# Performance work log

Measured on AMD Instinct MI355X. Metric: run time of the kernel, lower is better.

Reference implementation:

```python
import jax, jax.numpy as jnp
import numpy as np

H, DH = 8, 64  # num_heads, head_dim


def setup_inputs() -> dict:
    key = jax.random.key(0)
    ks = jax.random.split(key, 7)
    m, nq, nkv, d = 4, 2048, 2048, 512
    return {
        "xq": jax.random.normal(ks[0], (m, nq, d), jnp.float32),
        "xk": jax.random.normal(ks[1], (m, nkv, d), jnp.float32),
        "xv": jax.random.normal(ks[2], (m, nkv, d), jnp.float32),
        "Wq": jax.random.normal(ks[3], (d, H * DH), jnp.float32) * 0.02,
        "Wk": jax.random.normal(ks[4], (d, H * DH), jnp.float32) * 0.02,
        "Wv": jax.random.normal(ks[5], (d, H * DH), jnp.float32) * 0.02,
        "Wo": jax.random.normal(ks[6], (H * DH, d), jnp.float32) * 0.02,
        "bo": jnp.zeros((d,), jnp.float32),
    }


def _split_heads(t):
    # [b, n, h*d] -> [b, h, n, d]
    b, n, _ = t.shape
    return t.reshape(b, n, H, DH).transpose(0, 2, 1, 3)


def reference(xq, xk, xv, Wq, Wk, Wv, Wo, bo):
    scale = DH ** -0.5
    q = _split_heads(xq @ Wq)   # [b,h,nq,dh]
    k = _split_heads(xk @ Wk)   # [b,h,nkv,dh]
    v = _split_heads(xv @ Wv)   # [b,h,nkv,dh]
    dots = jnp.einsum("bhqd,bhkd->bhqk", q, k) * scale  # [b,h,nq,nkv]
    # diagonal attention term: query attends to its own (k,v) projection
    xq_k = _split_heads(xq @ Wk)
    xq_v = _split_heads(xq @ Wv)
    diag = jnp.sum(q * xq_k, axis=-1, keepdims=True) * scale  # [b,h,nq,1]
    dots = jnp.concatenate([dots, diag], axis=-1)  # [b,h,nq,nkv+1]
    attn = jax.nn.softmax(dots, axis=-1)
    out = jnp.einsum("bhqk,bhkd->bhqd", attn[..., :-1], v) + attn[..., -1:] * xq_v
    b, _, nq, _ = out.shape
    out = out.transpose(0, 2, 1, 3).reshape(b, nq, H * DH)  # merge heads
    return out @ Wo + bo
```

## Files before the change

### kernel.cpp

```cpp
#include <hip/hip_runtime.h>

#define LOG2E 1.44269504088896f
#define CS (0.125f * LOG2E)

typedef __bf16 bf16x8 __attribute__((ext_vector_type(8)));
typedef float f32x4 __attribute__((ext_vector_type(4)));
typedef unsigned short u16x8 __attribute__((ext_vector_type(8)));

#if __has_builtin(__builtin_amdgcn_exp2f)
#define fexp2(x) __builtin_amdgcn_exp2f(x)
#else
extern "C" __device__ float __ocml_native_exp2_f32(float);
#define fexp2(x) __ocml_native_exp2_f32(x)
#endif

__device__ __forceinline__ unsigned short f2bf(float f) {
  union { float f; unsigned int u; } v{f};
  unsigned int r = v.u + 0x7fffu + ((v.u >> 16) & 1u);
  return (unsigned short)(r >> 16);
}
__device__ __forceinline__ float bf2f(unsigned short u) {
  union { unsigned int u; float f; } v; v.u = ((unsigned int)u) << 16; return v.f;
}
__device__ __forceinline__ unsigned int pkr(float a, float b) {
  unsigned int ua = __builtin_bit_cast(unsigned int, a) + 0x8000u;
  unsigned int ub = __builtin_bit_cast(unsigned int, b) + 0x8000u;
  return __builtin_amdgcn_perm(ub, ua, 0x07060302);
}

typedef __attribute__((address_space(3))) unsigned int lds32_t;
typedef const __attribute__((address_space(1))) unsigned int glb32_t;
__device__ __forceinline__ void gld16(const unsigned short* g, unsigned short* l) {
  __builtin_amdgcn_global_load_lds((glb32_t*)(unsigned long long)g,
                                   (lds32_t*)(unsigned int)(unsigned long long)l,
                                   16, 0, 0);
}

__global__ __launch_bounds__(256) void conv_all(
    const float* __restrict__ xq, const float* __restrict__ xk, const float* __restrict__ xv,
    const float* __restrict__ Wq, const float* __restrict__ Wk,
    const float* __restrict__ Wv, const float* __restrict__ Wo,
    unsigned short* __restrict__ oxq, unsigned short* __restrict__ oxk, unsigned short* __restrict__ oxv,
    unsigned short* __restrict__ oWq, unsigned short* __restrict__ oWk,
    unsigned short* __restrict__ oWv, unsigned short* __restrict__ oWo) {
  __shared__ unsigned short T[64 * 65];
  const int blk = blockIdx.x;
  if (blk < 12288) {
    const int N4 = (8192 * 512) / 4;
    int idx = blk * 256 + threadIdx.x;
    const float* src; unsigned short* dst; int i;
    if (idx < N4)          { src = xq; dst = oxq; i = idx; }
    else if (idx < 2 * N4) { src = xk; dst = oxk; i = idx - N4; }
    else                   { src = xv; dst = oxv; i = idx - 2 * N4; }
    float4 v = ((const float4*)src)[i];
    ushort4 o; o.x = f2bf(v.x); o.y = f2bf(v.y); o.z = f2bf(v.z); o.w = f2bf(v.w);
    ((ushort4*)dst)[i] = o;
  } else {
    const int wblk = blk - 12288;
    const int wsel = wblk >> 6;
    const int tile = wblk & 63;
    const int tk = (tile >> 3) * 64, tn = (tile & 7) * 64;
    const float* src = (wsel == 0) ? Wq : (wsel == 1) ? Wk : (wsel == 2) ? Wv : Wo;
    unsigned short* dst = (wsel == 0) ? oWq : (wsel == 1) ? oWk : (wsel == 2) ? oWv : oWo;
    const float scale = (wsel == 0) ? CS : 1.0f;
    const int rr = threadIdx.x >> 4;
    const int cc = (threadIdx.x & 15) * 4;
#pragma unroll
    for (int i = 0; i < 4; i++) {
      int row = rr + i * 16;
      float4 v = *(const float4*)&src[(size_t)(tk + row) * 512 + tn + cc];
      T[(cc + 0) * 65 + row] = f2bf(v.x * scale);
      T[(cc + 1) * 65 + row] = f2bf(v.y * scale);
      T[(cc + 2) * 65 + row] = f2bf(v.z * scale);
      T[(cc + 3) * 65 + row] = f2bf(v.w * scale);
    }
    __syncthreads();
#pragma unroll
    for (int i = 0; i < 4; i++) {
      int n = rr + i * 16;
      ushort4 o;
      o.x = T[n * 65 + cc + 0]; o.y = T[n * 65 + cc + 1];
      o.z = T[n * 65 + cc + 2]; o.w = T[n * 65 + cc + 3];
      *(ushort4*)&dst[(size_t)(tn + n) * 512 + tk + cc] = o;
    }
  }
}

__device__ __forceinline__ void gemm_tile(
    const unsigned short* __restrict__ A, const unsigned short* __restrict__ Bt,
    int rowBlk, int colBlk, unsigned short* As, unsigned short* Bs, f32x4 (&acc)[4][4]) {
  const int t = threadIdx.x;
  const int lane = t & 63, c = lane & 15, g = lane >> 4;
  const int w = t >> 6;
  const int wm = w & 1, wn = w >> 1;
#pragma unroll
  for (int i = 0; i < 4; i++)
#pragma unroll
    for (int j = 0; j < 4; j++)
#pragma unroll
      for (int r = 0; r < 4; r++) acc[i][j][r] = 0.f;

  const int sr = t >> 2, sch = t & 3;
#define STAGE_PROJ(kkk, buf)                                                     \
  do {                                                                           \
    unsigned short* Ad = As + (buf) * (128 * 32);                                \
    unsigned short* Bd = Bs + (buf) * (128 * 32);                                \
    gld16(&A[(size_t)(rowBlk + sr) * 512 + (kkk) + sch * 8], &Ad[t * 8]);        \
    gld16(&Bt[(size_t)(colBlk + sr) * 512 + (kkk) + sch * 8], &Bd[t * 8]);       \
    gld16(&A[(size_t)(rowBlk + sr + 64) * 512 + (kkk) + sch * 8],                \
          &Ad[(t + 256) * 8]);                                                   \
    gld16(&Bt[(size_t)(colBlk + sr + 64) * 512 + (kkk) + sch * 8],               \
          &Bd[(t + 256) * 8]);                                                   \
  } while (0)

  STAGE_PROJ(0, 0);
  __syncthreads();

  for (int kt = 0; kt < 16; kt++) {
    if (kt < 15) STAGE_PROJ((kt + 1) * 32, (kt + 1) & 1);
    const unsigned short* Ac = As + (kt & 1) * (128 * 32);
    const unsigned short* Bc = Bs + (kt & 1) * (128 * 32);
    bf16x8 af[4], bfr[4];
#pragma unroll
    for (int i = 0; i < 4; i++)
      af[i] = __builtin_bit_cast(bf16x8, *(const u16x8*)&Ac[(wm * 64 + i * 16 + c) * 32 + g * 8]);
#pragma unroll
    for (int j = 0; j < 4; j++)
      bfr[j] = __builtin_bit_cast(bf16x8, *(const u16x8*)&Bc[(wn * 64 + j * 16 + c) * 32 + g * 8]);
#pragma unroll
    for (int i = 0; i < 4; i++)
#pragma unroll
      for (int j = 0; j < 4; j++)
        acc[i][j] = __builtin_amdgcn_mfma_f32_16x16x32_bf16(af[i], bfr[j], acc[i][j], 0, 0, 0);
    if (kt < 15) __syncthreads();
  }
#undef STAGE_PROJ
}

__global__ __launch_bounds__(256) void proj_all(
    const unsigned short* __restrict__ xq, const unsigned short* __restrict__ xk,
    const unsigned short* __restrict__ xv,
    const unsigned short* __restrict__ Wq, const unsigned short* __restrict__ Wk,
    const unsigned short* __restrict__ Wv,
    unsigned short* __restrict__ Qo, unsigned short* __restrict__ XKo,
    unsigned short* __restrict__ XVo, unsigned short* __restrict__ Ko,
    unsigned short* __restrict__ Vto) {
  __shared__ unsigned short As[2 * 128 * 32];
  __shared__ unsigned short Bs[2 * 128 * 32];
  const int rowBlk = blockIdx.x * 128;
  const int y = blockIdx.y;
  const unsigned short* A; const unsigned short* Bt; int colBlk; int mode;
  unsigned short* out;
  if (y < 12) {
    int wsel = y >> 2;
    A = xq; colBlk = (y & 3) * 128; mode = 0;
    Bt = (wsel == 0) ? Wq : (wsel == 1) ? Wk : Wv;
    out = (wsel == 0) ? Qo : (wsel == 1) ? XKo : XVo;
  } else if (y < 16) {
    A = xk; Bt = Wk; out = Ko; colBlk = (y - 12) * 128; mode = 0;
  } else {
    A = xv; Bt = Wv; out = Vto; colBlk = (y - 16) * 128; mode = 1;
  }
  f32x4 acc[4][4];
  gemm_tile(A, Bt, rowBlk, colBlk, As, Bs, acc);
  const int t = threadIdx.x;
  const int w = t >> 6, lane = t & 63, c = lane & 15, g = lane >> 4;
  const int wm = w & 1, wn = w >> 1;
  if (mode == 0) {
#pragma unroll
    for (int i = 0; i < 4; i++)
#pragma unroll
      for (int j = 0; j < 4; j++)
#pragma unroll
        for (int r = 0; r < 4; r++) {
          int row = rowBlk + wm * 64 + i * 16 + g * 4 + r;
          int col = colBlk + wn * 64 + j * 16 + c;
          out[(size_t)row * 512 + col] = f2bf(acc[i][j][r]);
        }
  } else {
#pragma unroll
    for (int i = 0; i < 4; i++) {
      int tok0 = rowBlk + wm * 64 + i * 16 + g * 4;
      int bb = tok0 >> 11, n0 = tok0 & 2047;
#pragma unroll
      for (int j = 0; j < 4; j++) {
        int col = colBlk + wn * 64 + j * 16 + c;
        int hh = col >> 6, dh = col & 63;
        ushort4 o;
        o.x = f2bf(acc[i][j][0]); o.y = f2bf(acc[i][j][1]);
        o.z = f2bf(acc[i][j][2]); o.w = f2bf(acc[i][j][3]);
        *(ushort4*)&out[((size_t)(bb * 8 + hh) * 64 + dh) * 2048 + n0] = o;
      }
    }
  }
}

__global__ __launch_bounds__(256) void gemm_out(
    const unsigned short* __restrict__ A, const unsigned short* __restrict__ Bt,
    float* __restrict__ out, const float* __restrict__ bias) {
  __shared__ unsigned short As[2 * 128 * 32];
  __shared__ unsigned short Bs[2 * 64 * 32];
  const int rowBlk = blockIdx.x * 128;
  const int colBlk = blockIdx.y * 64;
  const int t = threadIdx.x;
  const int lane = t & 63, c = lane & 15, g = lane >> 4;
  const int w = t >> 6;
  const int wm = w & 1, wn = w >> 1;
  f32x4 acc[4][2];
#pragma unroll
  for (int i = 0; i < 4; i++)
#pragma unroll
    for (int j = 0; j < 2; j++)
#pragma unroll
      for (int r = 0; r < 4; r++) acc[i][j][r] = 0.f;

  const int sr = t >> 2, sch = t & 3;
#define STAGE_OUT(kkk, buf)                                                      \
  do {                                                                           \
    unsigned short* Ad = As + (buf) * (128 * 32);                                \
    unsigned short* Bd = Bs + (buf) * (64 * 32);                                 \
    gld16(&A[(size_t)(rowBlk + sr) * 512 + (kkk) + sch * 8], &Ad[t * 8]);        \
    gld16(&A[(size_t)(rowBlk + sr + 64) * 512 + (kkk) + sch * 8],                \
          &Ad[(t + 256) * 8]);                                                   \
    gld16(&Bt[(size_t)(colBlk + sr) * 512 + (kkk) + sch * 8], &Bd[t * 8]);       \
  } while (0)

  STAGE_OUT(0, 0);
  __syncthreads();

  for (int kt = 0; kt < 16; kt++) {
    if (kt < 15) STAGE_OUT((kt + 1) * 32, (kt + 1) & 1);
    const unsigned short* Ac = As + (kt & 1) * (128 * 32);
    const unsigned short* Bc = Bs + (kt & 1) * (64 * 32);
    bf16x8 af[4], bfr[2];
#pragma unroll
    for (int i = 0; i < 4; i++)
      af[i] = __builtin_bit_cast(bf16x8, *(const u16x8*)&Ac[(wm * 64 + i * 16 + c) * 32 + g * 8]);
#pragma unroll
    for (int j = 0; j < 2; j++)
      bfr[j] = __builtin_bit_cast(bf16x8, *(const u16x8*)&Bc[(wn * 32 + j * 16 + c) * 32 + g * 8]);
#pragma unroll
    for (int i = 0; i < 4; i++)
#pragma unroll
      for (int j = 0; j < 2; j++)
        acc[i][j] = __builtin_amdgcn_mfma_f32_16x16x32_bf16(af[i], bfr[j], acc[i][j], 0, 0, 0);
    if (kt < 15) __syncthreads();
  }
#undef STAGE_OUT
#pragma unroll
  for (int i = 0; i < 4; i++)
#pragma unroll
    for (int j = 0; j < 2; j++)
#pragma unroll
      for (int r = 0; r < 4; r++) {
        int row = rowBlk + wm * 64 + i * 16 + g * 4 + r;
        int col = colBlk + wn * 32 + j * 16 + c;
        out[(size_t)row * 512 + col] = acc[i][j][r] + bias[col];
      }
}

__global__ __launch_bounds__(512, 4) void attn_kernel(
    const unsigned short* __restrict__ Q, const unsigned short* __restrict__ K,
    const unsigned short* __restrict__ Vt, const unsigned short* __restrict__ XK,
    const unsigned short* __restrict__ XV, unsigned short* __restrict__ O) {
  __shared__ unsigned short Ks[2][64 * 64];
  __shared__ unsigned short Vs[3][64 * 64];
  __shared__ unsigned short Ps[2][8][16 * 72];
  __shared__ float Scr[8][32];
  const int t = threadIdx.x;
  const int w = t >> 6, lane = t & 63, c = lane & 15, g = lane >> 4;
  const int id = blockIdx.x + 16 * (blockIdx.y + 8 * blockIdx.z);
  const int h = id & 7;
  const int jj = id >> 3;
  const int qt = jj & 15;
  const int b = jj >> 4;
  const size_t hb = (size_t)b * (2048 * 512) + h * 64;
  const size_t vhb = (size_t)(b * 8 + h) * 64 * 2048;
  const int qbase = qt * 128 + w * 16;

  const int sr = t >> 3, sch = t & 7;
  const int ssl = (sch ^ (sr & 7)) * 8;
  const size_t kgoff = hb + (size_t)sr * 512 + ssl;
  const size_t vgoff = vhb + (size_t)sr * 2048 + ssl;

  const int sw0 = ((g ^ (c & 7)) << 3);
  const int sw1 = (((g | 4) ^ (c & 7)) << 3);

  bf16x8 qf[2];
#pragma unroll
  for (int hf = 0; hf < 2; hf++)
    qf[hf] = __builtin_bit_cast(bf16x8,
        *(const u16x8*)&Q[hb + (size_t)(qbase + c) * 512 + hf * 32 + g * 8]);

  f32x4 accO[4];
  float lq = 0.f;
#pragma unroll
  for (int jd = 0; jd < 4; jd++)
#pragma unroll
    for (int r = 0; r < 4; r++) accO[jd][r] = 0.f;

  gld16(&K[kgoff], &Ks[0][t * 8]);
  gld16(&Vt[vgoff], &Vs[0][t * 8]);
  __syncthreads();

  gld16(&K[kgoff + (size_t)(64 * 512)], &Ks[1][t * 8]);
  gld16(&Vt[vgoff + 64], &Vs[1][t * 8]);
  {
    unsigned short* Pw = &Ps[0][w][0];
    f32x4 s[4];
    __builtin_amdgcn_s_setprio(1);
#pragma unroll
    for (int j = 0; j < 4; j++) {
      bf16x8 kf0 = __builtin_bit_cast(bf16x8, *(const u16x8*)&Ks[0][(j * 16 + c) * 64 + sw0]);
      bf16x8 kf1 = __builtin_bit_cast(bf16x8, *(const u16x8*)&Ks[0][(j * 16 + c) * 64 + sw1]);
      f32x4 z; z[0] = z[1] = z[2] = z[3] = 0.f;
      z = __builtin_amdgcn_mfma_f32_16x16x32_bf16(kf0, qf[0], z, 0, 0, 0);
      z = __builtin_amdgcn_mfma_f32_16x16x32_bf16(kf1, qf[1], z, 0, 0, 0);
      s[j] = z;
    }
    __builtin_amdgcn_s_setprio(0);
    float sum = 0.f;
#pragma unroll
    for (int j = 0; j < 4; j++) {
      float p0 = fexp2(s[j][0]);
      float p1 = fexp2(s[j][1]);
      float p2 = fexp2(s[j][2]);
      float p3 = fexp2(s[j][3]);
      sum += (p0 + p1) + (p2 + p3);
      uint2 pw; pw.x = pkr(p0, p1); pw.y = pkr(p2, p3);
      *(uint2*)&Pw[c * 72 + j * 16 + g * 4] = pw;
    }
    lq += sum;
  }
  __syncthreads();

  int vprev = 0, vcur = 1, vnext = 2;
  for (int kt = 1; kt < 32; kt++) {
    if (kt < 31) {
      gld16(&K[kgoff + (size_t)(kt + 1) * (64 * 512)], &Ks[(kt + 1) & 1][t * 8]);
      gld16(&Vt[vgoff + (size_t)(kt + 1) * 64], &Vs[vnext][t * 8]);
    }
    const unsigned short* Pp = &Ps[(kt - 1) & 1][w][0];
    bf16x8 pf0 = __builtin_bit_cast(bf16x8, *(const u16x8*)&Pp[c * 72 + g * 8]);
    bf16x8 pf1 = __builtin_bit_cast(bf16x8, *(const u16x8*)&Pp[c * 72 + 32 + g * 8]);

    const unsigned short* Kc = &Ks[kt & 1][0];
    f32x4 s[4];
    __builtin_amdgcn_s_setprio(1);
#pragma unroll
    for (int j = 0; j < 4; j++) {
      bf16x8 kf0 = __builtin_bit_cast(bf16x8, *(const u16x8*)&Kc[(j * 16 + c) * 64 + sw0]);
      bf16x8 kf1 = __builtin_bit_cast(bf16x8, *(const u16x8*)&Kc[(j * 16 + c) * 64 + sw1]);
      f32x4 z; z[0] = z[1] = z[2] = z[3] = 0.f;
      z = __builtin_amdgcn_mfma_f32_16x16x32_bf16(kf0, qf[0], z, 0, 0, 0);
      z = __builtin_amdgcn_mfma_f32_16x16x32_bf16(kf1, qf[1], z, 0, 0, 0);
      s[j] = z;
    }
    const unsigned short* Vc = &Vs[vprev][0];
#pragma unroll
    for (int jd = 0; jd < 4; jd++) {
      bf16x8 v0 = __builtin_bit_cast(bf16x8, *(const u16x8*)&Vc[(jd * 16 + c) * 64 + sw0]);
      bf16x8 v1 = __builtin_bit_cast(bf16x8, *(const u16x8*)&Vc[(jd * 16 + c) * 64 + sw1]);
      accO[jd] = __builtin_amdgcn_mfma_f32_16x16x32_bf16(pf0, v0, accO[jd], 0, 0, 0);
      accO[jd] = __builtin_amdgcn_mfma_f32_16x16x32_bf16(pf1, v1, accO[jd], 0, 0, 0);
    }
    __builtin_amdgcn_s_setprio(0);

    {
      unsigned short* Pw = &Ps[kt & 1][w][0];
      float sum = 0.f;
#pragma unroll
      for (int j = 0; j < 4; j++) {
        float p0 = fexp2(s[j][0]);
        float p1 = fexp2(s[j][1]);
        float p2 = fexp2(s[j][2]);
        float p3 = fexp2(s[j][3]);
        sum += (p0 + p1) + (p2 + p3);
        uint2 pw; pw.x = pkr(p0, p1); pw.y = pkr(p2, p3);
        *(uint2*)&Pw[c * 72 + j * 16 + g * 4] = pw;
      }
      lq += sum;
    }

    if (kt < 31) __syncthreads();
    int tmp = vprev; vprev = vcur; vcur = vnext; vnext = tmp;
  }

  {
    const unsigned short* Pp = &Ps[1][w][0];
    bf16x8 pf0 = __builtin_bit_cast(bf16x8, *(const u16x8*)&Pp[c * 72 + g * 8]);
    bf16x8 pf1 = __builtin_bit_cast(bf16x8, *(const u16x8*)&Pp[c * 72 + 32 + g * 8]);
    const unsigned short* Vc = &Vs[vprev][0];
    __builtin_amdgcn_s_setprio(1);
#pragma unroll
    for (int jd = 0; jd < 4; jd++) {
      bf16x8 v0 = __builtin_bit_cast(bf16x8, *(const u16x8*)&Vc[(jd * 16 + c) * 64 + sw0]);
      bf16x8 v1 = __builtin_bit_cast(bf16x8, *(const u16x8*)&Vc[(jd * 16 + c) * 64 + sw1]);
      accO[jd] = __builtin_amdgcn_mfma_f32_16x16x32_bf16(pf0, v0, accO[jd], 0, 0, 0);
      accO[jd] = __builtin_amdgcn_mfma_f32_16x16x32_bf16(pf1, v1, accO[jd], 0, 0, 0);
    }
    __builtin_amdgcn_s_setprio(0);
  }

  lq += __shfl_xor(lq, 16);
  lq += __shfl_xor(lq, 32);

  {
    const int qc = qbase + c;
    float part = 0.f;
    {
      const unsigned short* qp = &Q[hb + (size_t)qc * 512 + g * 16];
      const unsigned short* xp = &XK[hb + (size_t)qc * 512 + g * 16];
      u16x8 q0 = *(const u16x8*)&qp[0], q1 = *(const u16x8*)&qp[8];
      u16x8 x0 = *(const u16x8*)&xp[0], x1 = *(const u16x8*)&xp[8];
#pragma unroll
      for (int ii = 0; ii < 8; ii++)
        part += bf2f(q0[ii]) * bf2f(x0[ii]) + bf2f(q1[ii]) * bf2f(x1[ii]);
    }
    part += __shfl_xor(part, 16);
    part += __shfl_xor(part, 32);
    float pd = fexp2(part);
    float inv = 1.f / (lq + pd);
    if (g == 0) {
      Scr[w][c] = inv;
      Scr[w][16 + c] = pd * inv;
    }
    __builtin_amdgcn_s_waitcnt(0);
    f32x4 a4 = *(const f32x4*)&Scr[w][g * 4];
    f32x4 p4 = *(const f32x4*)&Scr[w][16 + g * 4];
#pragma unroll
    for (int jd = 0; jd < 4; jd++)
#pragma unroll
      for (int r = 0; r < 4; r++) {
        int qr = qbase + g * 4 + r;
        float xv = bf2f(XV[hb + (size_t)qr * 512 + jd * 16 + c]);
        float val = accO[jd][r] * a4[r] + p4[r] * xv;
        O[((size_t)(b * 2048 + qr)) * 512 + h * 64 + jd * 16 + c] = f2bf(val);
      }
  }
}

extern "C" void kernel_launch(void* const* d_in, const int* in_sizes, int n_in,
                              void* d_out, int out_size, void* d_ws, size_t ws_size,
                              hipStream_t stream) {
  const float* xq = (const float*)d_in[0];
  const float* xk = (const float*)d_in[1];
  const float* xv = (const float*)d_in[2];
  const float* Wq = (const float*)d_in[3];
  const float* Wk = (const float*)d_in[4];
  const float* Wv = (const float*)d_in[5];
  const float* Wo = (const float*)d_in[6];
  const float* bo = (const float*)d_in[7];

  unsigned short* ws = (unsigned short*)d_ws;
  const size_t MD = 8192ull * 512;
  const size_t WD = 512ull * 512;
  unsigned short* xq_b = ws;
  unsigned short* xk_b = xq_b + MD;
  unsigned short* xv_b = xk_b + MD;
  unsigned short* Wq_t = xv_b + MD;
  unsigned short* Wk_t = Wq_t + WD;
  unsigned short* Wv_t = Wk_t + WD;
  unsigned short* Wo_t = Wv_t + WD;
  unsigned short* Qb  = Wo_t + WD;
  unsigned short* Kb  = Qb + MD;
  unsigned short* Vtb = Kb + MD;
  unsigned short* XKb = Vtb + MD;
  unsigned short* XVb = XKb + MD;
  unsigned short* Ob  = XVb + MD;

  conv_all<<<dim3(12544), 256, 0, stream>>>(xq, xk, xv, Wq, Wk, Wv, Wo,
                                            xq_b, xk_b, xv_b, Wq_t, Wk_t, Wv_t, Wo_t);
  proj_all<<<dim3(64, 20), 256, 0, stream>>>(xq_b, xk_b, xv_b, Wq_t, Wk_t, Wv_t,
                                             Qb, XKb, XVb, Kb, Vtb);
  attn_kernel<<<dim3(16, 8, 4), 512, 0, stream>>>(Qb, Kb, Vtb, XKb, XVb, Ob);
  gemm_out<<<dim3(64, 8), 256, 0, stream>>>(Ob, Wo_t, (float*)d_out, bo);
}
```

Before: 202.4 us.

## Switch attention to 32x32 MFMA with register-resident P via permlane32 swap

Rewrites the attention kernel to use 32x32x16 bf16 MFMA, with each wave handling 32 query rows. The kernel now covers 256 queries per block, giving 256 blocks instead of 512. The P matrix stays in registers and is reshuffled with v_permlane32_swap instead of passing through LDS. This drops the software-pipelined P buffer and the triple-buffered V, removing LDS round trips and raising work per wave. The cost is more registers (launch bounds lowered to 2), less overlap of QK and PV, and only 256 blocks, which may underfill the GPU.

```diff
diff --git a/kernel.cpp b/kernel.cpp
--- a/kernel.cpp
+++ b/kernel.cpp
@@ -5,6 +5,7 @@
 
 typedef __bf16 bf16x8 __attribute__((ext_vector_type(8)));
 typedef float f32x4 __attribute__((ext_vector_type(4)));
+typedef float f32x16 __attribute__((ext_vector_type(16)));
 typedef unsigned short u16x8 __attribute__((ext_vector_type(8)));
 
 #if __has_builtin(__builtin_amdgcn_exp2f)
@@ -27,6 +28,8 @@
   unsigned int ub = __builtin_bit_cast(unsigned int, b) + 0x8000u;
   return __builtin_amdgcn_perm(ub, ua, 0x07060302);
 }
+
+#define PLSWAP(x, y) asm("v_permlane32_swap_b32 %0, %1" : "+v"(x), "+v"(y))
 
 typedef __attribute__((address_space(3))) unsigned int lds32_t;
 typedef const __attribute__((address_space(1))) unsigned int glb32_t;
@@ -259,185 +262,147 @@
       }
 }
 
-__global__ __launch_bounds__(512, 4) void attn_kernel(
+__global__ __launch_bounds__(512, 2) void attn_kernel(
     const unsigned short* __restrict__ Q, const unsigned short* __restrict__ K,
     const unsigned short* __restrict__ Vt, const unsigned short* __restrict__ XK,
     const unsigned short* __restrict__ XV, unsigned short* __restrict__ O) {
   __shared__ unsigned short Ks[2][64 * 64];
-  __shared__ unsigned short Vs[3][64 * 64];
-  __shared__ unsigned short Ps[2][8][16 * 72];
-  __shared__ float Scr[8][32];
+  __shared__ unsigned short Vs[2][64 * 64];
+  __shared__ float Fin[8][2][32];
   const int t = threadIdx.x;
-  const int w = t >> 6, lane = t & 63, c = lane & 15, g = lane >> 4;
-  const int id = blockIdx.x + 16 * (blockIdx.y + 8 * blockIdx.z);
-  const int h = id & 7;
-  const int jj = id >> 3;
-  const int qt = jj & 15;
-  const int b = jj >> 4;
+  const int w = t >> 6, lane = t & 63;
+  const int rowA = lane & 31, hi = lane >> 5, l7 = lane & 7;
+  const int id = blockIdx.x;
+  const int h = id & 7, qt = (id >> 3) & 7, b = id >> 6;
   const size_t hb = (size_t)b * (2048 * 512) + h * 64;
   const size_t vhb = (size_t)(b * 8 + h) * 64 * 2048;
-  const int qbase = qt * 128 + w * 16;
+  const int qb0 = qt * 256 + w * 32;
 
   const int sr = t >> 3, sch = t & 7;
   const int ssl = (sch ^ (sr & 7)) * 8;
   const size_t kgoff = hb + (size_t)sr * 512 + ssl;
   const size_t vgoff = vhb + (size_t)sr * 2048 + ssl;
 
-  const int sw0 = ((g ^ (c & 7)) << 3);
-  const int sw1 = (((g | 4) ^ (c & 7)) << 3);
-
-  bf16x8 qf[2];
-#pragma unroll
-  for (int hf = 0; hf < 2; hf++)
-    qf[hf] = __builtin_bit_cast(bf16x8,
-        *(const u16x8*)&Q[hb + (size_t)(qbase + c) * 512 + hf * 32 + g * 8]);
-
-  f32x4 accO[4];
+  bf16x8 qf[4];
+#pragma unroll
+  for (int d = 0; d < 4; d++)
+    qf[d] = __builtin_bit_cast(bf16x8,
+        *(const u16x8*)&Q[hb + (size_t)(qb0 + rowA) * 512 + d * 16 + hi * 8]);
+
+  f32x16 accO[2];
+#pragma unroll
+  for (int n = 0; n < 2; n++)
+#pragma unroll
+    for (int r = 0; r < 16; r++) accO[n][r] = 0.f;
   float lq = 0.f;
-#pragma unroll
-  for (int jd = 0; jd < 4; jd++)
-#pragma unroll
-    for (int r = 0; r < 4; r++) accO[jd][r] = 0.f;
 
   gld16(&K[kgoff], &Ks[0][t * 8]);
   gld16(&Vt[vgoff], &Vs[0][t * 8]);
   __syncthreads();
 
-  gld16(&K[kgoff + (size_t)(64 * 512)], &Ks[1][t * 8]);
-  gld16(&Vt[vgoff + 64], &Vs[1][t * 8]);
+  for (int kt = 0; kt < 32; kt++) {
+    const int cb = kt & 1;
+    if (kt < 31) {
+      gld16(&K[kgoff + (size_t)(kt + 1) * (64 * 512)], &Ks[cb ^ 1][t * 8]);
+      gld16(&Vt[vgoff + (size_t)(kt + 1) * 64], &Vs[cb ^ 1][t * 8]);
+    }
+    const unsigned short* Kc = &Ks[cb][0];
+    const unsigned short* Vc = &Vs[cb][0];
+
+    f32x16 s0, s1;
+#pragma unroll
+    for (int r = 0; r < 16; r++) { s0[r] = 0.f; s1[r] = 0.f; }
+    __builtin_amdgcn_s_setprio(1);
+#pragma unroll
+    for (int d = 0; d < 4; d++) {
+      bf16x8 k0 = __builtin_bit_cast(bf16x8,
+          *(const u16x8*)&Kc[rowA * 64 + (((d * 2 + hi) ^ l7) * 8)]);
+      s0 = __builtin_amdgcn_mfma_f32_32x32x16_bf16(k0, qf[d], s0, 0, 0, 0);
+    }
+#pragma unroll
+    for (int d = 0; d < 4; d++) {
+      bf16x8 k1 = __builtin_bit_cast(bf16x8,
+          *(const u16x8*)&Kc[(32 + rowA) * 64 + (((d * 2 + hi) ^ l7) * 8)]);
+      s1 = __builtin_amdgcn_mfma_f32_32x32x16_bf16(k1, qf[d], s1, 0, 0, 0);
+    }
+    __builtin_amdgcn_s_setprio(0);
+
+    float sum = 0.f;
+#pragma unroll
+    for (int r = 0; r < 16; r++) { s0[r] = fexp2(s0[r]); sum += s0[r]; }
+#pragma unroll
+    for (int r = 0; r < 16; r++) { s1[r] = fexp2(s1[r]); sum += s1[r]; }
+    lq += sum;
+
+#define PVSUB(P, T2)                                                            \
+  {                                                                             \
+    unsigned int x0 = pkr(P[0], P[1]),   y0 = pkr(P[4], P[5]);                  \
+    unsigned int x1 = pkr(P[2], P[3]),   y1 = pkr(P[6], P[7]);                  \
+    unsigned int x2 = pkr(P[8], P[9]),   y2 = pkr(P[12], P[13]);                \
+    unsigned int x3 = pkr(P[10], P[11]), y3 = pkr(P[14], P[15]);                \
+    PLSWAP(x0, y0); PLSWAP(x1, y1); PLSWAP(x2, y2); PLSWAP(x3, y3);             \
+    uint4 w0 = {x0, x1, y0, y1};                                                \
+    uint4 w1 = {x2, x3, y2, y3};                                                \
+    bf16x8 pa0 = __builtin_bit_cast(bf16x8, w0);                                \
+    bf16x8 pa1 = __builtin_bit_cast(bf16x8, w1);                                \
+    _Pragma("unroll")                                                           \
+    for (int n = 0; n < 2; n++) {                                               \
+      bf16x8 v0 = __builtin_bit_cast(bf16x8,                                    \
+          *(const u16x8*)&Vc[(n * 32 + rowA) * 64 + ((((T2) * 4 + hi) ^ l7) * 8)]); \
+      bf16x8 v1 = __builtin_bit_cast(bf16x8,                                    \
+          *(const u16x8*)&Vc[(n * 32 + rowA) * 64 + ((((T2) * 4 + 2 + hi) ^ l7) * 8)]); \
+      accO[n] = __builtin_amdgcn_mfma_f32_32x32x16_bf16(pa0, v0, accO[n], 0, 0, 0); \
+      accO[n] = __builtin_amdgcn_mfma_f32_32x32x16_bf16(pa1, v1, accO[n], 0, 0, 0); \
+    }                                                                           \
+  }
+    __builtin_amdgcn_s_setprio(1);
+    PVSUB(s0, 0);
+    PVSUB(s1, 1);
+    __builtin_amdgcn_s_setprio(0);
+#undef PVSUB
+
+    if (kt < 31) __syncthreads();
+  }
+
+  lq += __shfl_xor(lq, 32);
+
+  float part = 0.f;
   {
-    unsigned short* Pw = &Ps[0][w][0];
-    f32x4 s[4];
-    __builtin_amdgcn_s_setprio(1);
-#pragma unroll
-    for (int j = 0; j < 4; j++) {
-      bf16x8 kf0 = __builtin_bit_cast(bf16x8, *(const u16x8*)&Ks[0][(j * 16 + c) * 64 + sw0]);
-      bf16x8 kf1 = __builtin_bit_cast(bf16x8, *(const u16x8*)&Ks[0][(j * 16 + c) * 64 + sw1]);
-      f32x4 z; z[0] = z[1] = z[2] = z[3] = 0.f;
-      z = __builtin_amdgcn_mfma_f32_16x16x32_bf16(kf0, qf[0], z, 0, 0, 0);
-      z = __builtin_amdgcn_mfma_f32_16x16x32_bf16(kf1, qf[1], z, 0, 0, 0);
-      s[j] = z;
-    }
-    __builtin_amdgcn_s_setprio(0);
-    float sum = 0.f;
-#pragma unroll
-    for (int j = 0; j < 4; j++) {
-      float p0 = fexp2(s[j][0]);
-      float p1 = fexp2(s[j][1]);
-      float p2 = fexp2(s[j][2]);
-      float p3 = fexp2(s[j][3]);
-      sum += (p0 + p1) + (p2 + p3);
-      uint2 pw; pw.x = pkr(p0, p1); pw.y = pkr(p2, p3);
-      *(uint2*)&Pw[c * 72 + j * 16 + g * 4] = pw;
-    }
-    lq += sum;
-  }
-  __syncthreads();
-
-  int vprev = 0, vcur = 1, vnext = 2;
-  for (int kt = 1; kt < 32; kt++) {
-    if (kt < 31) {
-      gld16(&K[kgoff + (size_t)(kt + 1) * (64 * 512)], &Ks[(kt + 1) & 1][t * 8]);
-      gld16(&Vt[vgoff + (size_t)(kt + 1) * 64], &Vs[vnext][t * 8]);
-    }
-    const unsigned short* Pp = &Ps[(kt - 1) & 1][w][0];
-    bf16x8 pf0 = __builtin_bit_cast(bf16x8, *(const u16x8*)&Pp[c * 72 + g * 8]);
-    bf16x8 pf1 = __builtin_bit_cast(bf16x8, *(const u16x8*)&Pp[c * 72 + 32 + g * 8]);
-
-    const unsigned short* Kc = &Ks[kt & 1][0];
-    f32x4 s[4];
-    __builtin_amdgcn_s_setprio(1);
-#pragma unroll
-    for (int j = 0; j < 4; j++) {
-      bf16x8 kf0 = __builtin_bit_cast(bf16x8, *(const u16x8*)&Kc[(j * 16 + c) * 64 + sw0]);
-      bf16x8 kf1 = __builtin_bit_cast(bf16x8, *(const u16x8*)&Kc[(j * 16 + c) * 64 + sw1]);
-      f32x4 z; z[0] = z[1] = z[2] = z[3] = 0.f;
-      z = __builtin_amdgcn_mfma_f32_16x16x32_bf16(kf0, qf[0], z, 0, 0, 0);
-      z = __builtin_amdgcn_mfma_f32_16x16x32_bf16(kf1, qf[1], z, 0, 0, 0);
-      s[j] = z;
-    }
-    const unsigned short* Vc = &Vs[vprev][0];
-#pragma unroll
-    for (int jd = 0; jd < 4; jd++) {
-      bf16x8 v0 = __builtin_bit_cast(bf16x8, *(const u16x8*)&Vc[(jd * 16 + c) * 64 + sw0]);
-      bf16x8 v1 = __builtin_bit_cast(bf16x8, *(const u16x8*)&Vc[(jd * 16 + c) * 64 + sw1]);
-      accO[jd] = __builtin_amdgcn_mfma_f32_16x16x32_bf16(pf0, v0, accO[jd], 0, 0, 0);
-      accO[jd] = __builtin_amdgcn_mfma_f32_16x16x32_bf16(pf1, v1, accO[jd], 0, 0, 0);
-    }
-    __builtin_amdgcn_s_setprio(0);
-
-    {
-      unsigned short* Pw = &Ps[kt & 1][w][0];
-      float sum = 0.f;
-#pragma unroll
-      for (int j = 0; j < 4; j++) {
-        float p0 = fexp2(s[j][0]);
-        float p1 = fexp2(s[j][1]);
-        float p2 = fexp2(s[j][2]);
-        float p3 = fexp2(s[j][3]);
-        sum += (p0 + p1) + (p2 + p3);
-        uint2 pw; pw.x = pkr(p0, p1); pw.y = pkr(p2, p3);
-        *(uint2*)&Pw[c * 72 + j * 16 + g * 4] = pw;
-      }
-      lq += sum;
-    }
-
-    if (kt < 31) __syncthreads();
-    int tmp = vprev; vprev = vcur; vcur = vnext; vnext = tmp;
-  }
-
-  {
-    const unsigned short* Pp = &Ps[1][w][0];
-    bf16x8 pf0 = __builtin_bit_cast(bf16x8, *(const u16x8*)&Pp[c * 72 + g * 8]);
-    bf16x8 pf1 = __builtin_bit_cast(bf16x8, *(const u16x8*)&Pp[c * 72 + 32 + g * 8]);
-    const unsigned short* Vc = &Vs[vprev][0];
-    __builtin_amdgcn_s_setprio(1);
-#pragma unroll
-    for (int jd = 0; jd < 4; jd++) {
-      bf16x8 v0 = __builtin_bit_cast(bf16x8, *(const u16x8*)&Vc[(jd * 16 + c) * 64 + sw0]);
-      bf16x8 v1 = __builtin_bit_cast(bf16x8, *(const u16x8*)&Vc[(jd * 16 + c) * 64 + sw1]);
-      accO[jd] = __builtin_amdgcn_mfma_f32_16x16x32_bf16(pf0, v0, accO[jd], 0, 0, 0);
-      accO[jd] = __builtin_amdgcn_mfma_f32_16x16x32_bf16(pf1, v1, accO[jd], 0, 0, 0);
-    }
-    __builtin_amdgcn_s_setprio(0);
-  }
-
-  lq += __shfl_xor(lq, 16);
-  lq += __shfl_xor(lq, 32);
-
-  {
-    const int qc = qbase + c;
-    float part = 0.f;
-    {
-      const unsigned short* qp = &Q[hb + (size_t)qc * 512 + g * 16];
-      const unsigned short* xp = &XK[hb + (size_t)qc * 512 + g * 16];
-      u16x8 q0 = *(const u16x8*)&qp[0], q1 = *(const u16x8*)&qp[8];
-      u16x8 x0 = *(const u16x8*)&xp[0], x1 = *(const u16x8*)&xp[8];
-#pragma unroll
-      for (int ii = 0; ii < 8; ii++)
-        part += bf2f(q0[ii]) * bf2f(x0[ii]) + bf2f(q1[ii]) * bf2f(x1[ii]);
-    }
-    part += __shfl_xor(part, 16);
-    part += __shfl_xor(part, 32);
-    float pd = fexp2(part);
-    float inv = 1.f / (lq + pd);
-    if (g == 0) {
-      Scr[w][c] = inv;
-      Scr[w][16 + c] = pd * inv;
-    }
-    __builtin_amdgcn_s_waitcnt(0);
-    f32x4 a4 = *(const f32x4*)&Scr[w][g * 4];
-    f32x4 p4 = *(const f32x4*)&Scr[w][16 + g * 4];
-#pragma unroll
-    for (int jd = 0; jd < 4; jd++)
-#pragma unroll
-      for (int r = 0; r < 4; r++) {
-        int qr = qbase + g * 4 + r;
-        float xv = bf2f(XV[hb + (size_t)qr * 512 + jd * 16 + c]);
-        float val = accO[jd][r] * a4[r] + p4[r] * xv;
-        O[((size_t)(b * 2048 + qr)) * 512 + h * 64 + jd * 16 + c] = f2bf(val);
-      }
-  }
+    const size_t base = hb + (size_t)(qb0 + rowA) * 512 + hi * 32;
+#pragma unroll
+    for (int ii = 0; ii < 4; ii++) {
+      u16x8 q8 = *(const u16x8*)&Q[base + ii * 8];
+      u16x8 x8 = *(const u16x8*)&XK[base + ii * 8];
+#pragma unroll
+      for (int e = 0; e < 8; e++) part += bf2f(q8[e]) * bf2f(x8[e]);
+    }
+  }
+  part += __shfl_xor(part, 32);
+  float pd = fexp2(part);
+  float inv = 1.f / (lq + pd);
+  if (lane < 32) {
+    Fin[w][0][rowA] = inv;
+    Fin[w][1][rowA] = pd * inv;
+  }
+  __builtin_amdgcn_s_waitcnt(0);
+
+  f32x4 inva[4], pia[4];
+#pragma unroll
+  for (int rq = 0; rq < 4; rq++) {
+    inva[rq] = *(const f32x4*)&Fin[w][0][rq * 8 + hi * 4];
+    pia[rq]  = *(const f32x4*)&Fin[w][1][rq * 8 + hi * 4];
+  }
+#pragma unroll
+  for (int n = 0; n < 2; n++)
+#pragma unroll
+    for (int reg = 0; reg < 16; reg++) {
+      const int rq = reg >> 2, r = reg & 3;
+      const int q = rq * 8 + hi * 4 + r;
+      const int qrow = qb0 + q;
+      float xv = bf2f(XV[hb + (size_t)qrow * 512 + n * 32 + rowA]);
+      float val = accO[n][reg] * inva[rq][r] + pia[rq][r] * xv;
+      O[((size_t)(b * 2048 + qrow)) * 512 + h * 64 + n * 32 + rowA] = f2bf(val);
+    }
 }
 
 extern "C" void kernel_launch(void* const* d_in, const int* in_sizes, int n_in,
@@ -473,6 +438,6 @@
                                             xq_b, xk_b, xv_b, Wq_t, Wk_t, Wv_t, Wo_t);
   proj_all<<<dim3(64, 20), 256, 0, stream>>>(xq_b, xk_b, xv_b, Wq_t, Wk_t, Wv_t,
                                              Qb, XKb, XVb, Kb, Vtb);
-  attn_kernel<<<dim3(16, 8, 4), 512, 0, stream>>>(Qb, Kb, Vtb, XKb, XVb, Ob);
+  attn_kernel<<<dim3(256), 512, 0, stream>>>(Qb, Kb, Vtb, XKb, XVb, Ob);
   gemm_out<<<dim3(64, 8), 256, 0, stream>>>(Ob, Wo_t, (float*)d_out, bo);
 }
```

Measured after the change: 201.2 us. Within noise of the previous version (-0.6%).
